# Kernel tuning notes

Hardware: AMD Instinct MI355X
Metric: run time of the kernel (lower is better)

Reference implementation:

```python
import jax, jax.numpy as jnp
import numpy as np

SCOPE = 2
N = 20
D = 64
CAP = 32
IN_CH = 64
OUT_CH = 64
FIN_CH = 64
WIDTH = 2 * SCOPE + 1


def setup_inputs() -> dict:
    key = jax.random.key(0)
    ks = jax.random.split(key, 7)
    dm = 3 * CAP + D  # memory feature dim: 3 relpos blocks + spatial embedding

    def w(k, fan_in, shape):
        return jax.random.normal(k, shape, jnp.float32) / np.sqrt(fan_in)

    return dict(
        spatial_embeddings=jax.random.normal(ks[0], (N, N, N, D), jnp.float32),
        relpos_w=jax.random.normal(ks[1], (WIDTH, CAP), jnp.float32) / np.sqrt(WIDTH * CAP),
        Wq=w(ks[2], D, (D, IN_CH)), bq=jnp.zeros((IN_CH,), jnp.float32),
        Wk=w(ks[3], dm, (dm, IN_CH)), bk=jnp.zeros((IN_CH,), jnp.float32),
        Wv=w(ks[4], dm, (dm, OUT_CH)), bv=jnp.zeros((OUT_CH,), jnp.float32),
        Wo=w(ks[5], OUT_CH, (OUT_CH, FIN_CH)), bo=jnp.zeros((FIN_CH,), jnp.float32),
    )


def reference(spatial_embeddings, relpos_w, Wq, bq, Wk, bk, Wv, bv, Wo, bo):
    n = spatial_embeddings.shape[0]
    w = WIDTH
    m = n + 2 * SCOPE  # padded grid size
    cap = relpos_w.shape[-1]

    # within_edges=False: zero-pad all three spatial axes by SCOPE
    se = jnp.pad(spatial_embeddings, ((SCOPE, SCOPE),) * 3 + ((0, 0),))
    central = SCOPE + jnp.arange(n)               # padded centre indices [n]
    off = jnp.arange(-SCOPE, SCOPE + 1)           # [w]
    idx = central[:, None] + off[None, :]         # [n, w] padded neighbour indices

    # relative-position cube: relpos_cube[x,y,z] = concat(r[x], r[y], r[z])
    r0 = jnp.broadcast_to(relpos_w[:, None, None, :], (w, w, w, cap))
    r1 = jnp.broadcast_to(relpos_w[None, :, None, :], (w, w, w, cap))
    r2 = jnp.broadcast_to(relpos_w[None, None, :, :], (w, w, w, cap))
    relpos_flat = jnp.concatenate([r0, r1, r2], axis=-1).reshape(w * w * w, 3 * cap)

    # neighbour gather replicating jnp.meshgrid(...)'s default 'xy' indexing:
    # cube[b, a, c] = se[ni[a], nj[b], nk[c]]
    ii = idx[:, None, None, None, :, None]        # (qi, a)
    jj = idx[None, :, None, :, None, None]        # (qj, b)
    kk = idx[None, None, :, None, None, :]        # (qk, c)
    nb = se[ii, jj, kk]                           # [n,n,n,w,w,w,D]
    nb = nb.reshape(n, n, n, w * w * w, -1)       # [n,n,n,w^3,D]

    # keys/values over memory = concat(relpos, neighbours); split the weight
    Wk_rel, Wk_nb = Wk[:3 * cap], Wk[3 * cap:]
    Wv_rel, Wv_nb = Wv[:3 * cap], Wv[3 * cap:]
    k_rel = relpos_flat @ Wk_rel + bk             # [w^3, IN_CH] (query-independent)
    v_rel = relpos_flat @ Wv_rel + bv             # [w^3, OUT_CH]
    keys = k_rel + jnp.einsum('xyzpd,dc->xyzpc', nb, Wk_nb)
    values = v_rel + jnp.einsum('xyzpd,dc->xyzpc', nb, Wv_nb)

    # centre embedding at padded index `central` == original unpadded embedding
    q = spatial_embeddings @ Wq + bq              # [n,n,n,IN_CH]
    logits = jnp.einsum('xyzc,xyzpc->xyzp', q, keys)

    # edge mask, built in (a,b,c) cube order (faithful to original's flatten order)
    valid = ((idx > SCOPE) & (idx < m - SCOPE)).astype(logits.dtype)  # [n, w]
    mask = (valid[:, None, None, :, None, None]
            * valid[None, :, None, None, :, None]
            * valid[None, None, :, None, None, :]).reshape(n, n, n, w * w * w)
    logits = logits - (1.0 - mask) * 1e9

    scores = jax.nn.softmax(logits, axis=-1)
    reweighted = jnp.einsum('xyzp,xyzpc->xyzc', scores, values)
    return reweighted @ Wo + bo                   # [n,n,n,FIN_CH]
```

## Files before the change

kernel.cpp:

```cpp
#include <hip/hip_runtime.h>

#define NN 20
#define NP 125
#define NV (NN*NN*NN)

__device__ __forceinline__ float rlf(float v, int l) {
    return __uint_as_float(__builtin_amdgcn_readlane(__float_as_uint(v), l));
}

__global__ __launch_bounds__(64) void prep(
        const float* __restrict__ rpw,
        const float* __restrict__ Wk, const float* __restrict__ bk,
        const float* __restrict__ Wv, const float* __restrict__ bv,
        const float* __restrict__ Wo,
        float* __restrict__ k_rel, float* __restrict__ vrelW,
        float* __restrict__ Wvo) {
    const int c = threadIdx.x;
    if (blockIdx.x < NP) {
        const int p = blockIdx.x;
        const int d3 = p / 25, d4 = (p / 5) % 5, d5 = p % 5;
        __shared__ float vtmp[64];
        float ak = bk[c], av = bv[c];
#pragma unroll
        for (int t = 0; t < 96; ++t) {
            const int blk = t >> 5, off = t & 31;
            const int row = (blk == 0) ? d3 : (blk == 1) ? d4 : d5;
            const float r = rpw[row * 32 + off];
            ak = fmaf(r, Wk[t * 64 + c], ak);
            av = fmaf(r, Wv[t * 64 + c], av);
        }
        k_rel[p * 64 + c] = ak;
        vtmp[c] = av;
        __syncthreads();
        float o = 0.f;
#pragma unroll 8
        for (int e = 0; e < 64; ++e)
            o = fmaf(vtmp[e], Wo[e * 64 + c], o);
        vrelW[p * 64 + c] = o;
    } else {
        const int d = blockIdx.x - NP;
        float acc = 0.f;
#pragma unroll 8
        for (int e = 0; e < 64; ++e)
            acc = fmaf(Wv[(96 + d) * 64 + e], Wo[e * 64 + c], acc);
        Wvo[d * 64 + c] = acc;
    }
}

__global__ __launch_bounds__(256) void qkv3(
        const float* __restrict__ SE,
        const float* __restrict__ Wq, const float* __restrict__ bq,
        const float* __restrict__ Wk, const float* __restrict__ Wvo,
        const float* __restrict__ k_rel,
        float* __restrict__ Q, float* __restrict__ Km, float* __restrict__ VW,
        float* __restrict__ qkr) {
    __shared__ float se_s[32][65];
    __shared__ float krs[125 * 65];
    const int t = threadIdx.x;
    const int vbase = blockIdx.x * 32;
    {
        const float4* __restrict__ src = (const float4*)(SE + vbase * 64);
        const float4 a = src[t];
        const float4 b = src[t + 256];
        const int r0 = t >> 4,        c0 = (t & 15) * 4;
        const int r1 = (t + 256) >> 4;
        se_s[r0][c0 + 0] = a.x; se_s[r0][c0 + 1] = a.y;
        se_s[r0][c0 + 2] = a.z; se_s[r0][c0 + 3] = a.w;
        se_s[r1][c0 + 0] = b.x; se_s[r1][c0 + 1] = b.y;
        se_s[r1][c0 + 2] = b.z; se_s[r1][c0 + 3] = b.w;
    }
    for (int i = t; i < 125 * 16; i += 256) {
        const int row = i >> 4, ch = i & 15;
        const float4 val = ((const float4*)k_rel)[row * 16 + ch];
        const int b = row * 65 + ch * 4;
        krs[b] = val.x; krs[b + 1] = val.y; krs[b + 2] = val.z; krs[b + 3] = val.w;
    }
    __syncthreads();
    const int lane = t & 63, w = t >> 6;
    float aq[8], ak[8], av[8];
#pragma unroll
    for (int j = 0; j < 8; ++j) { aq[j] = bq[lane]; ak[j] = 0.f; av[j] = 0.f; }
#pragma unroll 8
    for (int d = 0; d < 64; ++d) {
        const float wq = Wq[d * 64 + lane];
        const float wk = Wk[(96 + d) * 64 + lane];
        const float wv = Wvo[d * 64 + lane];
#pragma unroll
        for (int j = 0; j < 8; ++j) {
            const float s = se_s[w * 8 + j][d];
            aq[j] = fmaf(s, wq, aq[j]);
            ak[j] = fmaf(s, wk, ak[j]);
            av[j] = fmaf(s, wv, av[j]);
        }
    }
#pragma unroll
    for (int j = 0; j < 8; ++j) {
        const int v = vbase + w * 8 + j;
        Q[v * 64 + lane]  = aq[j];
        Km[v * 64 + lane] = ak[j];
        VW[v * 64 + lane] = av[j];
    }
    const int p1c = (lane + 64 < NP) ? (lane + 64) : (NP - 1);
#pragma unroll
    for (int j = 0; j < 8; ++j) {
        float d0 = 0.f, d1 = 0.f;
#pragma unroll
        for (int i = 0; i < 16; ++i) {
            const float qa = rlf(aq[j], 4 * i + 0);
            const float qb = rlf(aq[j], 4 * i + 1);
            const float qc = rlf(aq[j], 4 * i + 2);
            const float qd = rlf(aq[j], 4 * i + 3);
            const int b0 = lane * 65 + 4 * i;
            const int b1 = p1c * 65 + 4 * i;
            d0 = fmaf(krs[b0], qa, d0); d0 = fmaf(krs[b0 + 1], qb, d0);
            d0 = fmaf(krs[b0 + 2], qc, d0); d0 = fmaf(krs[b0 + 3], qd, d0);
            d1 = fmaf(krs[b1], qa, d1); d1 = fmaf(krs[b1 + 1], qb, d1);
            d1 = fmaf(krs[b1 + 2], qc, d1); d1 = fmaf(krs[b1 + 3], qd, d1);
        }
        const int v = vbase + w * 8 + j;
        qkr[v * 128 + lane] = d0;
        qkr[v * 128 + 64 + lane] = d1;
    }
}

__global__ __launch_bounds__(512, 2) void attn7(
        const float* __restrict__ Q, const float* __restrict__ Km,
        const float* __restrict__ VW, const float* __restrict__ qkr,
        const float* __restrict__ vrelW, const float* __restrict__ bo,
        float* __restrict__ out) {
    __shared__ __align__(16) float u[216 * 68];

    const int tid  = threadIdx.x;
    const int lane = tid & 63;
    const int w    = tid >> 6;

    const int chunk = blockIdx.x & 7;
    const int idx   = blockIdx.x >> 3;
    const int cx = chunk >> 2, cy = (chunk >> 1) & 1, cz = chunk & 1;
    const int TX = cx * 5 + idx / 25;
    const int TY = cy * 5 + (idx / 5) % 5;
    const int TZ = cz * 5 + idx % 5;

    const int wx = w >> 2, wy = (w >> 1) & 1, wz = w & 1;
    const int x = TX * 2 + wx, y = TY * 2 + wy, z = TZ * 2 + wz;
    const int v = (x * NN + y) * NN + z;

    for (int i = tid; i < 216 * 16; i += 512) {
        const int row = i >> 4, ch = i & 15;
        const int ux = row / 36, uy = (row / 6) % 6, uz = row % 6;
        const int gX = TX * 2 - 2 + ux;
        const int gY = TY * 2 - 2 + uy;
        const int gZ = TZ * 2 - 2 + uz;
        float4 val = make_float4(0.f, 0.f, 0.f, 0.f);
        if ((unsigned)gX <= 19u && (unsigned)gY <= 19u && (unsigned)gZ <= 19u)
            val = ((const float4*)Km)[((gX * NN + gY) * NN + gZ) * 16 + ch];
        *(float4*)&u[row * 68 + ch * 4] = val;
    }

    const float q = Q[v * 64 + lane];

    int   rr0, rr1, rr2, rr3;
    float qk0, qk1, qk2, qk3;
    bool  vd0, vd1, vd2, vd3;
#define GEO(M, RR, QK, VD)                                                     \
    {                                                                          \
        const int r = lane + 64 * (M);                                         \
        const bool okr = (r < 216);                                            \
        const int rc = okr ? r : 0;                                            \
        const int ux = rc / 36, uy = (rc / 6) % 6, uz = rc % 6;                \
        const int E4 = ux - wx, E3 = uy - wy, E5 = uz - wz;                    \
        const bool win = okr && (unsigned)E3 <= 4u && (unsigned)E4 <= 4u &&    \
                         (unsigned)E5 <= 4u;                                   \
        const bool mv = win && (unsigned)(x + E3 - 3) <= 18u &&                \
                        (unsigned)(y + E4 - 3) <= 18u &&                       \
                        (unsigned)(z + E5 - 3) <= 18u;                         \
        const int p = 25 * E3 + 5 * E4 + E5;                                   \
        RR = rc; VD = mv;                                                      \
        QK = qkr[v * 128 + (mv ? p : 0)];                                      \
    }
    GEO(0, rr0, qk0, vd0)
    GEO(1, rr1, qk1, vd1)
    GEO(2, rr2, qk2, vd2)
    GEO(3, rr3, qk3, vd3)
#undef GEO

    __syncthreads();

    float a0 = 0.f, a1 = 0.f, a2 = 0.f, a3 = 0.f;
#pragma unroll
    for (int i = 0; i < 16; ++i) {
        const float qa = rlf(q, 4 * i + 0);
        const float qb = rlf(q, 4 * i + 1);
        const float qc = rlf(q, 4 * i + 2);
        const float qd = rlf(q, 4 * i + 3);
        const float4 k0 = *(const float4*)&u[rr0 * 68 + 4 * i];
        const float4 k1 = *(const float4*)&u[rr1 * 68 + 4 * i];
        const float4 k2 = *(const float4*)&u[rr2 * 68 + 4 * i];
        const float4 k3 = *(const float4*)&u[rr3 * 68 + 4 * i];
        a0 = fmaf(k0.x, qa, a0); a0 = fmaf(k0.y, qb, a0);
        a0 = fmaf(k0.z, qc, a0); a0 = fmaf(k0.w, qd, a0);
        a1 = fmaf(k1.x, qa, a1); a1 = fmaf(k1.y, qb, a1);
        a1 = fmaf(k1.z, qc, a1); a1 = fmaf(k1.w, qd, a1);
        a2 = fmaf(k2.x, qa, a2); a2 = fmaf(k2.y, qb, a2);
        a2 = fmaf(k2.z, qc, a2); a2 = fmaf(k2.w, qd, a2);
        a3 = fmaf(k3.x, qa, a3); a3 = fmaf(k3.y, qb, a3);
        a3 = fmaf(k3.z, qc, a3); a3 = fmaf(k3.w, qd, a3);
    }
    const float l0 = vd0 ? a0 + qk0 : -1e9f;
    const float l1 = vd1 ? a1 + qk1 : -1e9f;
    const float l2 = vd2 ? a2 + qk2 : -1e9f;
    const float l3 = vd3 ? a3 + qk3 : -1e9f;

    float mm = fmaxf(fmaxf(l0, l1), fmaxf(l2, l3));
#pragma unroll
    for (int d = 1; d < 64; d <<= 1) mm = fmaxf(mm, __shfl_xor(mm, d));
    const float e0 = __expf(l0 - mm);
    const float e1 = __expf(l1 - mm);
    const float e2 = __expf(l2 - mm);
    const float e3v = __expf(l3 - mm);
    float ss = ((e0 + e1) + (e2 + e3v));
#pragma unroll
    for (int d = 1; d < 64; d <<= 1) ss += __shfl_xor(ss, d);
    const float inv = 1.f / ss;
    const float sA = e0 * inv, sB = e1 * inv, sC = e2 * inv, sD = e3v * inv;

    int d3 = lane / 25, d4 = (lane / 5) % 5, d5 = lane % 5;
    const int r0 = 36 * (wx + d4) + 6 * (wy + d3) + (wz + d5);
    const int p1c = (lane + 64 < NP) ? (lane + 64) : (NP - 1);
    d3 = p1c / 25; d4 = (p1c / 5) % 5; d5 = p1c % 5;
    const int r1 = 36 * (wx + d4) + 6 * (wy + d3) + (wz + d5);
    const float cA0 = __shfl(sA, r0 & 63), cB0 = __shfl(sB, r0 & 63);
    const float cC0 = __shfl(sC, r0 & 63), cD0 = __shfl(sD, r0 & 63);
    const int sl0 = r0 >> 6;
    const float s0 = (sl0 == 0) ? cA0 : (sl0 == 1) ? cB0 : (sl0 == 2) ? cC0 : cD0;
    const float cA1 = __shfl(sA, r1 & 63), cB1 = __shfl(sB, r1 & 63);
    const float cC1 = __shfl(sC, r1 & 63), cD1 = __shfl(sD, r1 & 63);
    const int sl1 = r1 >> 6;
    const float s1 = (sl1 == 0) ? cA1 : (sl1 == 1) ? cB1 : (sl1 == 2) ? cC1 : cD1;

    __syncthreads();

    for (int i = tid; i < 216 * 16; i += 512) {
        const int row = i >> 4, ch = i & 15;
        const int ux = row / 36, uy = (row / 6) % 6, uz = row % 6;
        const int gX = TX * 2 - 2 + ux;
        const int gY = TY * 2 - 2 + uy;
        const int gZ = TZ * 2 - 2 + uz;
        float4 val = make_float4(0.f, 0.f, 0.f, 0.f);
        if ((unsigned)gX <= 19u && (unsigned)gY <= 19u && (unsigned)gZ <= 19u)
            val = ((const float4*)VW)[((gX * NN + gY) * NN + gZ) * 16 + ch];
        *(float4*)&u[row * 68 + ch * 4] = val;
    }
    __syncthreads();

    float A0 = 0.f, A1 = 0.f, A2 = 0.f, A3 = 0.f, A4 = 0.f;
    const float* __restrict__ vr = vrelW + lane;
#pragma unroll 5
    for (int g = 0; g < 25; ++g) {
        const int ge3 = g / 5, ge4 = g % 5;
        const int rb = 36 * (wx + ge4) + 6 * (wy + ge3) + wz;
        const int pb = g * 5;
#define STEP(J, ACC)                                                           \
        {                                                                      \
            const int p = pb + (J);                                            \
            const float sc = (p < 64) ? rlf(s0, p) : rlf(s1, p - 64);          \
            ACC = fmaf(sc, u[(rb + (J)) * 68 + lane] + vr[p * 64], ACC);       \
        }
        STEP(0, A0) STEP(1, A1) STEP(2, A2) STEP(3, A3) STEP(4, A4)
#undef STEP
    }
    const float rw = ((A0 + A1) + (A2 + A3)) + A4;
    out[v * 64 + lane] = rw + bo[lane];
}

extern "C" void kernel_launch(void* const* d_in, const int* in_sizes, int n_in,
                              void* d_out, int out_size, void* d_ws, size_t ws_size,
                              hipStream_t stream) {
    const float* SE  = (const float*)d_in[0];
    const float* rpw = (const float*)d_in[1];
    const float* Wq  = (const float*)d_in[2];
    const float* bq  = (const float*)d_in[3];
    const float* Wk  = (const float*)d_in[4];
    const float* bk  = (const float*)d_in[5];
    const float* Wv  = (const float*)d_in[6];
    const float* bv  = (const float*)d_in[7];
    const float* Wo  = (const float*)d_in[8];
    const float* bo  = (const float*)d_in[9];
    float* out = (float*)d_out;

    float* ws    = (float*)d_ws;
    float* Q     = ws;
    float* Km    = ws + 512000;
    float* VW    = ws + 1024000;
    float* k_rel = ws + 1536000;
    float* vrelW = ws + 1544000;
    float* Wvo   = ws + 1552000;
    float* qkr   = ws + 1556096;

    prep<<<NP + 64, 64, 0, stream>>>(rpw, Wk, bk, Wv, bv, Wo, k_rel, vrelW, Wvo);
    qkv3<<<NV / 32, 256, 0, stream>>>(SE, Wq, bq, Wk, Wvo, k_rel, Q, Km, VW, qkr);
    attn7<<<1000, 512, 0, stream>>>(Q, Km, VW, qkr, vrelW, bo, out);
}
```

Baseline: 137.6 us.

## Compute relative-position logits inside attention kernel instead of precomputing in qkv

Result: slower. 169.6 us (+23.3%).

```diff
diff --git a/kernel.cpp b/kernel.cpp
--- a/kernel.cpp
+++ b/kernel.cpp
@@ -47,15 +47,12 @@
     }
 }
 
-__global__ __launch_bounds__(256) void qkv3(
+__global__ __launch_bounds__(256) void qkv2(
         const float* __restrict__ SE,
         const float* __restrict__ Wq, const float* __restrict__ bq,
         const float* __restrict__ Wk, const float* __restrict__ Wvo,
-        const float* __restrict__ k_rel,
-        float* __restrict__ Q, float* __restrict__ Km, float* __restrict__ VW,
-        float* __restrict__ qkr) {
+        float* __restrict__ Q, float* __restrict__ Km, float* __restrict__ VW) {
     __shared__ float se_s[32][65];
-    __shared__ float krs[125 * 65];
     const int t = threadIdx.x;
     const int vbase = blockIdx.x * 32;
     {
@@ -69,12 +66,6 @@
         se_s[r1][c0 + 0] = b.x; se_s[r1][c0 + 1] = b.y;
         se_s[r1][c0 + 2] = b.z; se_s[r1][c0 + 3] = b.w;
     }
-    for (int i = t; i < 125 * 16; i += 256) {
-        const int row = i >> 4, ch = i & 15;
-        const float4 val = ((const float4*)k_rel)[row * 16 + ch];
-        const int b = row * 65 + ch * 4;
-        krs[b] = val.x; krs[b + 1] = val.y; krs[b + 2] = val.z; krs[b + 3] = val.w;
-    }
     __syncthreads();
     const int lane = t & 63, w = t >> 6;
     float aq[8], ak[8], av[8];
@@ -100,33 +91,13 @@
         Km[v * 64 + lane] = ak[j];
         VW[v * 64 + lane] = av[j];
     }
-    const int p1c = (lane + 64 < NP) ? (lane + 64) : (NP - 1);
-#pragma unroll
-    for (int j = 0; j < 8; ++j) {
-        float d0 = 0.f, d1 = 0.f;
-#pragma unroll
-        for (int i = 0; i < 16; ++i) {
-            const float qa = rlf(aq[j], 4 * i + 0);
-            const float qb = rlf(aq[j], 4 * i + 1);
-            const float qc = rlf(aq[j], 4 * i + 2);
-            const float qd = rlf(aq[j], 4 * i + 3);
-            const int b0 = lane * 65 + 4 * i;
-            const int b1 = p1c * 65 + 4 * i;
-            d0 = fmaf(krs[b0], qa, d0); d0 = fmaf(krs[b0 + 1], qb, d0);
-            d0 = fmaf(krs[b0 + 2], qc, d0); d0 = fmaf(krs[b0 + 3], qd, d0);
-            d1 = fmaf(krs[b1], qa, d1); d1 = fmaf(krs[b1 + 1], qb, d1);
-            d1 = fmaf(krs[b1 + 2], qc, d1); d1 = fmaf(krs[b1 + 3], qd, d1);
-        }
-        const int v = vbase + w * 8 + j;
-        qkr[v * 128 + lane] = d0;
-        qkr[v * 128 + 64 + lane] = d1;
-    }
-}
-
-__global__ __launch_bounds__(512, 2) void attn7(
+}
+
+__global__ __launch_bounds__(512, 2) void attn8(
         const float* __restrict__ Q, const float* __restrict__ Km,
-        const float* __restrict__ VW, const float* __restrict__ qkr,
-        const float* __restrict__ vrelW, const float* __restrict__ bo,
+        const float* __restrict__ VW,
+        const float* __restrict__ k_rel, const float* __restrict__ vrelW,
+        const float* __restrict__ bo,
         float* __restrict__ out) {
     __shared__ __align__(16) float u[216 * 68];
 
@@ -159,10 +130,10 @@
 
     const float q = Q[v * 64 + lane];
 
-    int   rr0, rr1, rr2, rr3;
-    float qk0, qk1, qk2, qk3;
-    bool  vd0, vd1, vd2, vd3;
-#define GEO(M, RR, QK, VD)                                                     \
+    int  rr0, rr1, rr2, rr3;
+    int  pc0, pc1, pc2, pc3;
+    bool vd0, vd1, vd2, vd3;
+#define GEO(M, RR, PC, VD)                                                     \
     {                                                                          \
         const int r = lane + 64 * (M);                                         \
         const bool okr = (r < 216);                                            \
@@ -174,15 +145,36 @@
         const bool mv = win && (unsigned)(x + E3 - 3) <= 18u &&                \
                         (unsigned)(y + E4 - 3) <= 18u &&                       \
                         (unsigned)(z + E5 - 3) <= 18u;                         \
-        const int p = 25 * E3 + 5 * E4 + E5;                                   \
         RR = rc; VD = mv;                                                      \
-        QK = qkr[v * 128 + (mv ? p : 0)];                                      \
-    }
-    GEO(0, rr0, qk0, vd0)
-    GEO(1, rr1, qk1, vd1)
-    GEO(2, rr2, qk2, vd2)
-    GEO(3, rr3, qk3, vd3)
+        PC = mv ? (25 * E3 + 5 * E4 + E5) : 0;                                 \
+    }
+    GEO(0, rr0, pc0, vd0)
+    GEO(1, rr1, pc1, vd1)
+    GEO(2, rr2, pc2, vd2)
+    GEO(3, rr3, pc3, vd3)
 #undef GEO
+
+    float qk0 = 0.f, qk1 = 0.f, qk2 = 0.f, qk3 = 0.f;
+    const float4* __restrict__ KR = (const float4*)k_rel;
+#pragma unroll
+    for (int i = 0; i < 16; ++i) {
+        const float qa = rlf(q, 4 * i + 0);
+        const float qb = rlf(q, 4 * i + 1);
+        const float qc = rlf(q, 4 * i + 2);
+        const float qd = rlf(q, 4 * i + 3);
+        const float4 k0 = KR[pc0 * 16 + i];
+        const float4 k1 = KR[pc1 * 16 + i];
+        const float4 k2 = KR[pc2 * 16 + i];
+        const float4 k3 = KR[pc3 * 16 + i];
+        qk0 = fmaf(k0.x, qa, qk0); qk0 = fmaf(k0.y, qb, qk0);
+        qk0 = fmaf(k0.z, qc, qk0); qk0 = fmaf(k0.w, qd, qk0);
+        qk1 = fmaf(k1.x, qa, qk1); qk1 = fmaf(k1.y, qb, qk1);
+        qk1 = fmaf(k1.z, qc, qk1); qk1 = fmaf(k1.w, qd, qk1);
+        qk2 = fmaf(k2.x, qa, qk2); qk2 = fmaf(k2.y, qb, qk2);
+        qk2 = fmaf(k2.z, qc, qk2); qk2 = fmaf(k2.w, qd, qk2);
+        qk3 = fmaf(k3.x, qa, qk3); qk3 = fmaf(k3.y, qb, qk3);
+        qk3 = fmaf(k3.z, qc, qk3); qk3 = fmaf(k3.w, qd, qk3);
+    }
 
     __syncthreads();
 
@@ -295,9 +287,8 @@
     float* k_rel = ws + 1536000;
     float* vrelW = ws + 1544000;
     float* Wvo   = ws + 1552000;
-    float* qkr   = ws + 1556096;
 
     prep<<<NP + 64, 64, 0, stream>>>(rpw, Wk, bk, Wv, bv, Wo, k_rel, vrelW, Wvo);
-    qkv3<<<NV / 32, 256, 0, stream>>>(SE, Wq, bq, Wk, Wvo, k_rel, Q, Km, VW, qkr);
-    attn7<<<1000, 512, 0, stream>>>(Q, Km, VW, qkr, vrelW, bo, out);
-}
+    qkv2<<<NV / 32, 256, 0, stream>>>(SE, Wq, bq, Wk, Wvo, Q, Km, VW);
+    attn8<<<1000, 512, 0, stream>>>(Q, Km, VW, k_rel, vrelW, bo, out);
+}
```
